# Kernel tuning notes

Measured on AMD Instinct MI355X. Metric: run time of the kernel, lower is better.

## Reference

```python
import jax, jax.numpy as jnp
import numpy as np
import math

B, L, D, H = 16, 512, 128, 8


def setup_inputs() -> dict:
    key = jax.random.key(0)
    ks = jax.random.split(key, 10)
    xavier = lambda k, shp: jax.random.normal(k, shp, jnp.float32) * math.sqrt(2.0 / (shp[0] + shp[1]))
    inp = {
        "x": jax.random.normal(ks[0], (B, L, D), jnp.float32),
        "W_q": xavier(ks[1], (H * D, D)),
        "b_q": jnp.zeros((H * D,), jnp.float32),
        "W_k": xavier(ks[2], (H * D, D)),
        "b_k": jnp.zeros((H * D,), jnp.float32),
        "W_v": xavier(ks[3], (H * D, D)),
        "b_v": jnp.zeros((H * D,), jnp.float32),
        "W_o": xavier(ks[4], (D, H * D)),
        "b_o": jnp.zeros((D,), jnp.float32),
        "pad_mask": jax.random.randint(ks[5], (B, L, L), 0, 2).astype(bool),
        "batch_size": B,
        "max_len": L,
    }
    return inp


def reference(x, W_q, b_q, W_k, b_k, W_v, b_v, W_o, b_o, pad_mask, batch_size, max_len):
    # project: [B, L, D] -> [B, L, H*D] -> head-major [H*B, L, D]
    def proj(W, b):
        y = jnp.einsum('bld,ed->ble', x, W) + b          # [B, L, H*D]
        y = y.reshape(batch_size, max_len, H, D)
        return y.transpose(2, 0, 1, 3).reshape(H * batch_size, max_len, D)

    q = proj(W_q, b_q)
    k = proj(W_k, b_k)
    v = proj(W_v, b_v)

    scores = jnp.einsum('nqd,nkd->nqk', q, k)            # [H*B, L, L]
    mask = jnp.tile(pad_mask, (H, 1, 1))                 # repeat(n_heads,1,1)
    # faithful quirk: mask BEFORE scaling, softmax over QUERY axis (dim=1)
    scores = jnp.where(mask, -1e9, scores) / math.sqrt(D)
    attn = jax.nn.softmax(scores, axis=1)
    att = jnp.einsum('nqk,nkd->nqd', attn, v)            # [H*B, L, D]
    # faithful quirk: torch .view from (H*B, L, D) to (B, L, H*D)
    att = att.reshape(batch_size, max_len, H * D)
    out = jnp.einsum('ble,de->bld', att, W_o) + b_o      # [B, L, D]
    return out
```

## Files before the change

kernel.cpp:

```cpp
#include <hip/hip_runtime.h>

#define B_  16
#define L_  512
#define D_  128
#define H_  8
#define HD_ 1024
#define NH_ 128
#define M_  8192

typedef unsigned short u16;
typedef __attribute__((ext_vector_type(8))) short s16x8;
typedef __attribute__((ext_vector_type(4))) float f32x4;

__device__ __forceinline__ float bf2f(u16 u) {
    union { unsigned u; float f; } x; x.u = ((unsigned)u) << 16; return x.f;
}
__device__ __forceinline__ u16 f2bf(float f) {
    unsigned u = __float_as_uint(f);
    return (u16)((u + 0x7FFFu + ((u >> 16) & 1u)) >> 16);
}

template<int MI, int MJ>
__device__ __forceinline__ void mfma_bt(const u16* __restrict__ A, int lda,
                                        const u16* __restrict__ B, int ldb,
                                        int K, int lane, f32x4 acc[MI][MJ]) {
    const int mr = lane & 15, quad = lane >> 4;
    for (int k0 = 0; k0 < K; k0 += 32) {
        s16x8 av[MI], bv[MJ];
#pragma unroll
        for (int i = 0; i < MI; i++)
            av[i] = *(const s16x8*)(A + (size_t)(i * 16 + mr) * lda + k0 + quad * 8);
#pragma unroll
        for (int j = 0; j < MJ; j++)
            bv[j] = *(const s16x8*)(B + (size_t)(j * 16 + mr) * ldb + k0 + quad * 8);
#pragma unroll
        for (int i = 0; i < MI; i++)
#pragma unroll
            for (int j = 0; j < MJ; j++)
                acc[i][j] = __builtin_amdgcn_mfma_f32_16x16x32_bf16(av[i], bv[j], acc[i][j], 0, 0, 0);
    }
}

__global__ void k0_detect(const unsigned int* __restrict__ pad,
                          const unsigned int* __restrict__ xw,
                          int* __restrict__ flags) {
    __shared__ int sMask, sCnt;
    if (threadIdx.x == 0) { sMask = 0; sCnt = 0; }
    __syncthreads();
    int bad = 0;
#pragma unroll
    for (int i = 0; i < 4; i++) {
        unsigned u = pad[threadIdx.x * 4 + i];
        bad |= (u > 1u) ? 1 : 0;
    }
    int cnt = 0;
#pragma unroll
    for (int i = 0; i < 16; i++) {
        unsigned w = xw[threadIdx.x * 16 + i];
        unsigned e = (w >> 7) & 0xFFu;
        cnt += (e >= 100u && e <= 131u) ? 1 : 0;
    }
    if (bad) atomicOr(&sMask, 1);
    atomicAdd(&sCnt, cnt);
    __syncthreads();
    if (threadIdx.x == 0) {
        flags[0] = (sCnt > 2048) ? 1 : 0;
        flags[1] = sMask;
    }
}

#define PREP_G8 197008
__global__ __launch_bounds__(256) void kprep_conv8(
    const void* x, const void* Wq, const void* bq, const void* Wk, const void* bk,
    const void* Wv, const void* bv, const void* Wo, const void* bo,
    const int* __restrict__ flags,
    u16* xb, u16* Wqb, u16* Wkb, u16* Wvb, u16* Wob,
    u16* bqb, u16* bkb, u16* bvb, u16* bob) {
    int g = blockIdx.x * 256 + threadIdx.x;
    if (g >= PREP_G8) return;
    int e0 = g * 8;
    const int dt = flags[0];
    const void* src; u16* dst; int off;
    if      (e0 < 1048576) { src = x;  dst = xb;  off = e0; }
    else if (e0 < 1179648) { src = Wq; dst = Wqb; off = e0 - 1048576; }
    else if (e0 < 1310720) { src = Wk; dst = Wkb; off = e0 - 1179648; }
    else if (e0 < 1441792) { src = Wv; dst = Wvb; off = e0 - 1310720; }
    else if (e0 < 1572864) { src = Wo; dst = Wob; off = e0 - 1441792; }
    else if (e0 < 1573888) { src = bq; dst = bqb; off = e0 - 1572864; }
    else if (e0 < 1574912) { src = bk; dst = bkb; off = e0 - 1573888; }
    else if (e0 < 1575936) { src = bv; dst = bvb; off = e0 - 1574912; }
    else                   { src = bo; dst = bob; off = e0 - 1575936; }
    if (dt) {
        *(uint4*)(dst + off) = *(const uint4*)((const u16*)src + off);
    } else {
        float4 a = *(const float4*)((const float*)src + off);
        float4 b = *(const float4*)((const float*)src + off + 4);
        u16 t[8] = {f2bf(a.x), f2bf(a.y), f2bf(a.z), f2bf(a.w),
                    f2bf(b.x), f2bf(b.y), f2bf(b.z), f2bf(b.w)};
        *(uint4*)(dst + off) = *(const uint4*)t;
    }
}

__global__ __launch_bounds__(256) void kprep_mask(const void* __restrict__ pad,
                                                  const int* __restrict__ flags,
                                                  unsigned* __restrict__ mb,
                                                  float* __restrict__ lsum) {
    int w = blockIdx.x * 256 + threadIdx.x;
    if (w < 65536) lsum[w] = 0.f;
    unsigned m = 0;
    if (flags[1]) {
        union { uint4 v[2]; unsigned a[8]; } u;
        u.v[0] = ((const uint4*)pad)[w * 2];
        u.v[1] = ((const uint4*)pad)[w * 2 + 1];
#pragma unroll
        for (int b = 0; b < 32; b++)
            m |= (((u.a[b >> 2] >> ((b & 3) * 8)) & 0xFFu) ? 1u : 0u) << b;
    } else {
        union { uint4 v[8]; unsigned a[32]; } u;
#pragma unroll
        for (int i = 0; i < 8; i++) u.v[i] = ((const uint4*)pad)[w * 8 + i];
#pragma unroll
        for (int b = 0; b < 32; b++) m |= (u.a[b] ? 1u : 0u) << b;
    }
    mb[w] = m;
}

__global__ __launch_bounds__(256) void k1_proj(
    const u16* __restrict__ xb,
    const u16* __restrict__ Wqb, const u16* __restrict__ Wkb, const u16* __restrict__ Wvb,
    const u16* __restrict__ bqb, const u16* __restrict__ bkb, const u16* __restrict__ bvb,
    u16* __restrict__ qb, u16* __restrict__ kb, u16* __restrict__ vtb) {
    const int h  = blockIdx.x;
    const int m0 = blockIdx.y * 128;
    const int z  = blockIdx.z;
    const u16* W    = (z == 0) ? Wqb : (z == 1) ? Wkb : Wvb;
    const u16* bias = (z == 0) ? bqb : (z == 1) ? bkb : bvb;

    const int lane = threadIdx.x & 63, wave = threadIdx.x >> 6;
    const int wr = wave >> 1, wc = wave & 1;
    const int mr = lane & 15, quad = lane >> 4;

    f32x4 acc[4][4];
#pragma unroll
    for (int i = 0; i < 4; i++)
#pragma unroll
        for (int j = 0; j < 4; j++) acc[i][j] = (f32x4){0.f, 0.f, 0.f, 0.f};

    mfma_bt<4,4>(xb + (size_t)(m0 + wr * 64) * D_, D_,
                 W + (size_t)(h * 128 + wc * 64) * D_, D_, D_, lane, acc);

    __shared__ __align__(16) u16 T[128][136];
#pragma unroll
    for (int i = 0; i < 4; i++)
#pragma unroll
        for (int j = 0; j < 4; j++) {
            int col = wc * 64 + j * 16 + mr;
            float bv_ = bf2f(bias[h * 128 + col]);
#pragma unroll
            for (int r = 0; r < 4; r++)
                T[wr * 64 + i * 16 + quad * 4 + r][col] = f2bf(acc[i][j][r] + bv_);
        }
    __syncthreads();

    const int bb = m0 >> 9, l0 = m0 & 511;
    const int t = threadIdx.x;
    if (z < 2) {
        u16* out = z ? kb : qb;
        int row = t >> 1, c0 = (t & 1) * 64;
        u16* dst = out + ((size_t)(h * B_ + bb) * L_ + l0 + row) * D_ + c0;
#pragma unroll
        for (int c = 0; c < 64; c += 8)
            *(uint4*)(dst + c) = *(const uint4*)&T[row][c0 + c];
    } else {
        int d = t >> 1, lc0 = (t & 1) * 64;
        u16* dst = vtb + ((size_t)(h * B_ + bb) * D_ + d) * L_ + l0 + lc0;
#pragma unroll
        for (int c = 0; c < 64; c += 8) {
            u16 tmp[8];
#pragma unroll
            for (int s = 0; s < 8; s++) tmp[s] = T[lc0 + c + s][d];
            *(uint4*)(dst + c) = *(const uint4*)tmp;
        }
    }
}

__global__ __launch_bounds__(256) void k2_escore(
    const u16* __restrict__ qb, const u16* __restrict__ kb,
    const unsigned* __restrict__ mbits,
    u16* __restrict__ E, float* __restrict__ lsum) {
    const int n  = blockIdx.x;
    const int ks = blockIdx.y;
    const int qq = blockIdx.z;
    const int bb = n & (B_ - 1);
    const int tid = threadIdx.x;
    const int lane = tid & 63, wave = tid >> 6;
    const int wr = wave >> 1, wc = wave & 1;
    const int mr = lane & 15, quad = lane >> 4;
    const float rs = 0.08838834764831845f;

    __shared__ __align__(16) u16 Te[128][136];
    __shared__ unsigned mw[512];
    __shared__ float CS[2][128];

#pragma unroll
    for (int s = 0; s < 2; s++) {
        int idx = tid * 2 + s;
        int ql = idx >> 2, lw = idx & 3;
        mw[idx] = mbits[((size_t)(bb << 9) + qq * 128 + ql) * 16 + ks * 4 + lw];
    }
    __syncthreads();

    f32x4 acc[4][4];
#pragma unroll
    for (int i = 0; i < 4; i++)
#pragma unroll
        for (int j = 0; j < 4; j++) acc[i][j] = (f32x4){0.f, 0.f, 0.f, 0.f};

    mfma_bt<4,4>(qb + (size_t)n * L_ * D_ + (size_t)(qq * 128 + wr * 64) * D_, D_,
                 kb + (size_t)n * L_ * D_ + (size_t)(ks * 128 + wc * 64) * D_, D_,
                 D_, lane, acc);

    float colsum[4] = {0.f, 0.f, 0.f, 0.f};
#pragma unroll
    for (int j = 0; j < 4; j++) {
        const int kc = wc * 64 + j * 16 + mr;
        const int lw = kc >> 5, bit = kc & 31;
#pragma unroll
        for (int i = 0; i < 4; i++)
#pragma unroll
            for (int r = 0; r < 4; r++) {
                int ql = wr * 64 + i * 16 + quad * 4 + r;
                float e = ((mw[(ql << 2) + lw] >> bit) & 1u)
                          ? 0.f : __expf(acc[i][j][r] * rs);
                colsum[j] += e;
                Te[ql][kc] = f2bf(e);
            }
    }
#pragma unroll
    for (int j = 0; j < 4; j++) {
        colsum[j] += __shfl_xor(colsum[j], 16);
        colsum[j] += __shfl_xor(colsum[j], 32);
    }
    if (quad == 0) {
#pragma unroll
        for (int j = 0; j < 4; j++) CS[wr][wc * 64 + j * 16 + mr] = colsum[j];
    }
    __syncthreads();

    {
        int row = tid >> 1, c0 = (tid & 1) * 64;
        u16* dst = E + ((size_t)(n * L_ + qq * 128 + row)) * L_ + ks * 128 + c0;
#pragma unroll
        for (int c = 0; c < 64; c += 8)
            *(uint4*)(dst + c) = *(const uint4*)&Te[row][c0 + c];
    }
    if (tid < 128)
        atomicAdd(&lsum[(size_t)n * L_ + ks * 128 + tid], CS[0][tid] + CS[1][tid]);
}

__global__ __launch_bounds__(256) void k3_vscale(u16* __restrict__ vtb,
                                                 const float* __restrict__ lsum) {
    int idx = blockIdx.x * 256 + threadIdx.x;
    int n = idx >> 13;
    int rem = idx & 8191;
    int d = rem >> 6;
    int kg = (rem & 63) << 3;
    u16* p = vtb + ((size_t)n * D_ + d) * L_ + kg;
    uint4 v = *(const uint4*)p;
    float4 l0 = *(const float4*)(lsum + (size_t)n * L_ + kg);
    float4 l1 = *(const float4*)(lsum + (size_t)n * L_ + kg + 4);
    float lv[8] = {1.f/l0.x, 1.f/l0.y, 1.f/l0.z, 1.f/l0.w,
                   1.f/l1.x, 1.f/l1.y, 1.f/l1.z, 1.f/l1.w};
    u16* u = (u16*)&v;
#pragma unroll
    for (int s = 0; s < 8; s++) u[s] = f2bf(bf2f(u[s]) * lv[s]);
    *(uint4*)p = v;
}

__global__ __launch_bounds__(256) void k4_av(
    const u16* __restrict__ E, const u16* __restrict__ vtb,
    u16* __restrict__ att) {
    const int n  = blockIdx.x;
    const int qt = blockIdx.y;
    const int tid = threadIdx.x;
    const int lane = tid & 63, w = tid >> 6;
    const int mr = lane & 15, quad = lane >> 4;

    f32x4 acc[4][2];
#pragma unroll
    for (int i = 0; i < 4; i++)
#pragma unroll
        for (int j = 0; j < 2; j++) acc[i][j] = (f32x4){0.f, 0.f, 0.f, 0.f};

    mfma_bt<4,2>(E + ((size_t)n * L_ + qt * 64) * L_, L_,
                 vtb + ((size_t)n * D_ + w * 32) * L_, L_, L_, lane, acc);

    __shared__ __align__(16) u16 Ta[64][136];
#pragma unroll
    for (int i = 0; i < 4; i++)
#pragma unroll
        for (int j = 0; j < 2; j++) {
            int col = w * 32 + j * 16 + mr;
#pragma unroll
            for (int r = 0; r < 4; r++)
                Ta[i * 16 + quad * 4 + r][col] = f2bf(acc[i][j][r]);
        }
    __syncthreads();
    int row = tid >> 2, c0 = (tid & 3) * 32;
    u16* dst = att + ((size_t)(n * L_ + qt * 64 + row)) * D_ + c0;
#pragma unroll
    for (int c = 0; c < 32; c += 8)
        *(uint4*)(dst + c) = *(const uint4*)&Ta[row][c0 + c];
}

__global__ __launch_bounds__(256) void k5_out(
    const u16* __restrict__ att, const u16* __restrict__ Wob,
    const u16* __restrict__ bob, const int* __restrict__ flags,
    void* __restrict__ out) {
    const int dt = flags[0];
    const int n0 = blockIdx.x * 64;
    const int m0 = blockIdx.y * 32;
    const int tid = threadIdx.x;
    const int lane = tid & 63, wk = tid >> 6;
    const int mr = lane & 15, quad = lane >> 4;

    f32x4 acc[2][4];
#pragma unroll
    for (int i = 0; i < 2; i++)
#pragma unroll
        for (int j = 0; j < 4; j++) acc[i][j] = (f32x4){0.f, 0.f, 0.f, 0.f};

    mfma_bt<2,4>(att + (size_t)m0 * HD_ + wk * 256, HD_,
                 Wob + (size_t)n0 * HD_ + wk * 256, HD_, 256, lane, acc);

    __shared__ __align__(16) float Tf[2][32][68];
    if (wk < 2) {
#pragma unroll
        for (int i = 0; i < 2; i++)
#pragma unroll
            for (int j = 0; j < 4; j++)
#pragma unroll
                for (int r = 0; r < 4; r++)
                    Tf[wk][i * 16 + quad * 4 + r][j * 16 + mr] = acc[i][j][r];
    }
    __syncthreads();
    if (wk >= 2) {
#pragma unroll
        for (int i = 0; i < 2; i++)
#pragma unroll
            for (int j = 0; j < 4; j++)
#pragma unroll
                for (int r = 0; r < 4; r++)
                    Tf[wk - 2][i * 16 + quad * 4 + r][j * 16 + mr] += acc[i][j][r];
    }
    __syncthreads();

    int row = tid >> 3, c0 = (tid & 7) * 8;
    size_t base = (size_t)(m0 + row) * D_ + n0 + c0;
    float v[8];
#pragma unroll
    for (int s = 0; s < 8; s++)
        v[s] = Tf[0][row][c0 + s] + Tf[1][row][c0 + s] + bf2f(bob[n0 + c0 + s]);
    if (dt) {
        u16 tmp[8];
#pragma unroll
        for (int s = 0; s < 8; s++) tmp[s] = f2bf(v[s]);
        *(uint4*)((u16*)out + base) = *(const uint4*)tmp;
    } else {
        float* o = (float*)out;
        *(float4*)(o + base)     = *(const float4*)&v[0];
        *(float4*)(o + base + 4) = *(const float4*)&v[4];
    }
}

extern "C" void kernel_launch(void* const* d_in, const int* in_sizes, int n_in,
                              void* d_out, int out_size, void* d_ws, size_t ws_size,
                              hipStream_t stream) {
    (void)in_sizes; (void)n_in; (void)out_size; (void)ws_size;
    const void* x  = d_in[0];
    const void* Wq = d_in[1]; const void* bq = d_in[2];
    const void* Wk = d_in[3]; const void* bk = d_in[4];
    const void* Wv = d_in[5]; const void* bv = d_in[6];
    const void* Wo = d_in[7]; const void* bo = d_in[8];
    const void* pad = d_in[9];

    char* p = (char*)d_ws;
    auto alloc = [&](size_t bytes) { char* r = p; p += (bytes + 255) & ~(size_t)255; return r; };
    int*  flags = (int*)alloc(256);
    u16*  xb   = (u16*)alloc(2097152);
    u16*  Wqb  = (u16*)alloc(262144);
    u16*  Wkb  = (u16*)alloc(262144);
    u16*  Wvb  = (u16*)alloc(262144);
    u16*  Wob  = (u16*)alloc(262144);
    u16*  bqb  = (u16*)alloc(2048);
    u16*  bkb  = (u16*)alloc(2048);
    u16*  bvb  = (u16*)alloc(2048);
    u16*  bob  = (u16*)alloc(256);
    unsigned* mbits = (unsigned*)alloc(524288);
    float* lsum = (float*)alloc(262144);
    u16*  qb   = (u16*)alloc(16777216);
    u16*  kb   = (u16*)alloc(16777216);
    u16*  vtb  = (u16*)alloc(16777216);
    u16*  E    = (u16*)alloc(67108864);
    u16*  att  = qb;

    k0_detect<<<1, 256, 0, stream>>>((const unsigned*)pad, (const unsigned*)x, flags);
    kprep_conv8<<<(PREP_G8 + 255) / 256, 256, 0, stream>>>(
        x, Wq, bq, Wk, bk, Wv, bv, Wo, bo, flags,
        xb, Wqb, Wkb, Wvb, Wob, bqb, bkb, bvb, bob);
    kprep_mask<<<512, 256, 0, stream>>>(pad, flags, mbits, lsum);
    k1_proj<<<dim3(8, 64, 3), 256, 0, stream>>>(
        xb, Wqb, Wkb, Wvb, bqb, bkb, bvb, qb, kb, vtb);
    k2_escore<<<dim3(128, 4, 4), 256, 0, stream>>>(qb, kb, mbits, E, lsum);
    k3_vscale<<<4096, 256, 0, stream>>>(vtb, lsum);
    k4_av<<<dim3(128, 8), 256, 0, stream>>>(E, vtb, att);
    k5_out<<<dim3(2, 256), 256, 0, stream>>>(att, Wob, bob, flags, d_out);
}
```

Baseline: 263.3 us.

## Fuse prep kernels, fold V column scaling into AV GEMM, retile score kernel

```diff
diff --git a/kernel.cpp b/kernel.cpp
--- a/kernel.cpp
+++ b/kernel.cpp
@@ -20,11 +20,12 @@
     return (u16)((u + 0x7FFFu + ((u >> 16) & 1u)) >> 16);
 }
 
-template<int MI, int MJ>
+template<int MI, int MJ, int K>
 __device__ __forceinline__ void mfma_bt(const u16* __restrict__ A, int lda,
                                         const u16* __restrict__ B, int ldb,
-                                        int K, int lane, f32x4 acc[MI][MJ]) {
+                                        int lane, f32x4 acc[MI][MJ]) {
     const int mr = lane & 15, quad = lane >> 4;
+#pragma unroll
     for (int k0 = 0; k0 < K; k0 += 32) {
         s16x8 av[MI], bv[MJ];
 #pragma unroll
@@ -70,59 +71,57 @@
 }
 
 #define PREP_G8 197008
-__global__ __launch_bounds__(256) void kprep_conv8(
+__global__ __launch_bounds__(256) void kprep(
     const void* x, const void* Wq, const void* bq, const void* Wk, const void* bk,
     const void* Wv, const void* bv, const void* Wo, const void* bo,
-    const int* __restrict__ flags,
+    const void* __restrict__ pad, const int* __restrict__ flags,
     u16* xb, u16* Wqb, u16* Wkb, u16* Wvb, u16* Wob,
-    u16* bqb, u16* bkb, u16* bvb, u16* bob) {
-    int g = blockIdx.x * 256 + threadIdx.x;
-    if (g >= PREP_G8) return;
-    int e0 = g * 8;
-    const int dt = flags[0];
-    const void* src; u16* dst; int off;
-    if      (e0 < 1048576) { src = x;  dst = xb;  off = e0; }
-    else if (e0 < 1179648) { src = Wq; dst = Wqb; off = e0 - 1048576; }
-    else if (e0 < 1310720) { src = Wk; dst = Wkb; off = e0 - 1179648; }
-    else if (e0 < 1441792) { src = Wv; dst = Wvb; off = e0 - 1310720; }
-    else if (e0 < 1572864) { src = Wo; dst = Wob; off = e0 - 1441792; }
-    else if (e0 < 1573888) { src = bq; dst = bqb; off = e0 - 1572864; }
-    else if (e0 < 1574912) { src = bk; dst = bkb; off = e0 - 1573888; }
-    else if (e0 < 1575936) { src = bv; dst = bvb; off = e0 - 1574912; }
-    else                   { src = bo; dst = bob; off = e0 - 1575936; }
-    if (dt) {
-        *(uint4*)(dst + off) = *(const uint4*)((const u16*)src + off);
+    u16* bqb, u16* bkb, u16* bvb, u16* bob,
+    unsigned* __restrict__ mb, float* __restrict__ lsum) {
+    if (blockIdx.x < 770) {
+        int g = blockIdx.x * 256 + threadIdx.x;
+        if (g >= PREP_G8) return;
+        int e0 = g * 8;
+        const int dt = flags[0];
+        const void* src; u16* dst; int off;
+        if      (e0 < 1048576) { src = x;  dst = xb;  off = e0; }
+        else if (e0 < 1179648) { src = Wq; dst = Wqb; off = e0 - 1048576; }
+        else if (e0 < 1310720) { src = Wk; dst = Wkb; off = e0 - 1179648; }
+        else if (e0 < 1441792) { src = Wv; dst = Wvb; off = e0 - 1310720; }
+        else if (e0 < 1572864) { src = Wo; dst = Wob; off = e0 - 1441792; }
+        else if (e0 < 1573888) { src = bq; dst = bqb; off = e0 - 1572864; }
+        else if (e0 < 1574912) { src = bk; dst = bkb; off = e0 - 1573888; }
+        else if (e0 < 1575936) { src = bv; dst = bvb; off = e0 - 1574912; }
+        else                   { src = bo; dst = bob; off = e0 - 1575936; }
+        if (dt) {
+            *(uint4*)(dst + off) = *(const uint4*)((const u16*)src + off);
+        } else {
+            float4 a = *(const float4*)((const float*)src + off);
+            float4 b = *(const float4*)((const float*)src + off + 4);
+            u16 t[8] = {f2bf(a.x), f2bf(a.y), f2bf(a.z), f2bf(a.w),
+                        f2bf(b.x), f2bf(b.y), f2bf(b.z), f2bf(b.w)};
+            *(uint4*)(dst + off) = *(const uint4*)t;
+        }
     } else {
-        float4 a = *(const float4*)((const float*)src + off);
-        float4 b = *(const float4*)((const float*)src + off + 4);
-        u16 t[8] = {f2bf(a.x), f2bf(a.y), f2bf(a.z), f2bf(a.w),
-                    f2bf(b.x), f2bf(b.y), f2bf(b.z), f2bf(b.w)};
-        *(uint4*)(dst + off) = *(const uint4*)t;
-    }
-}
-
-__global__ __launch_bounds__(256) void kprep_mask(const void* __restrict__ pad,
-                                                  const int* __restrict__ flags,
-                                                  unsigned* __restrict__ mb,
-                                                  float* __restrict__ lsum) {
-    int w = blockIdx.x * 256 + threadIdx.x;
-    if (w < 65536) lsum[w] = 0.f;
-    unsigned m = 0;
-    if (flags[1]) {
-        union { uint4 v[2]; unsigned a[8]; } u;
-        u.v[0] = ((const uint4*)pad)[w * 2];
-        u.v[1] = ((const uint4*)pad)[w * 2 + 1];
-#pragma unroll
-        for (int b = 0; b < 32; b++)
-            m |= (((u.a[b >> 2] >> ((b & 3) * 8)) & 0xFFu) ? 1u : 0u) << b;
-    } else {
-        union { uint4 v[8]; unsigned a[32]; } u;
-#pragma unroll
-        for (int i = 0; i < 8; i++) u.v[i] = ((const uint4*)pad)[w * 8 + i];
-#pragma unroll
-        for (int b = 0; b < 32; b++) m |= (u.a[b] ? 1u : 0u) << b;
-    }
-    mb[w] = m;
+        int w = (blockIdx.x - 770) * 256 + threadIdx.x;
+        if (w < 65536) lsum[w] = 0.f;
+        unsigned m = 0;
+        if (flags[1]) {
+            union { uint4 v[2]; unsigned a[8]; } u;
+            u.v[0] = ((const uint4*)pad)[w * 2];
+            u.v[1] = ((const uint4*)pad)[w * 2 + 1];
+#pragma unroll
+            for (int b = 0; b < 32; b++)
+                m |= (((u.a[b >> 2] >> ((b & 3) * 8)) & 0xFFu) ? 1u : 0u) << b;
+        } else {
+            union { uint4 v[8]; unsigned a[32]; } u;
+#pragma unroll
+            for (int i = 0; i < 8; i++) u.v[i] = ((const uint4*)pad)[w * 8 + i];
+#pragma unroll
+            for (int b = 0; b < 32; b++) m |= (u.a[b] ? 1u : 0u) << b;
+        }
+        mb[w] = m;
+    }
 }
 
 __global__ __launch_bounds__(256) void k1_proj(
@@ -146,8 +145,8 @@
 #pragma unroll
         for (int j = 0; j < 4; j++) acc[i][j] = (f32x4){0.f, 0.f, 0.f, 0.f};
 
-    mfma_bt<4,4>(xb + (size_t)(m0 + wr * 64) * D_, D_,
-                 W + (size_t)(h * 128 + wc * 64) * D_, D_, D_, lane, acc);
+    mfma_bt<4,4,128>(xb + (size_t)(m0 + wr * 64) * D_, D_,
+                     W + (size_t)(h * 128 + wc * 64) * D_, D_, lane, acc);
 
     __shared__ __align__(16) u16 T[128][136];
 #pragma unroll
@@ -190,112 +189,116 @@
     u16* __restrict__ E, float* __restrict__ lsum) {
     const int n  = blockIdx.x;
     const int ks = blockIdx.y;
-    const int qq = blockIdx.z;
+    const int qs = blockIdx.z;
     const int bb = n & (B_ - 1);
     const int tid = threadIdx.x;
-    const int lane = tid & 63, wave = tid >> 6;
-    const int wr = wave >> 1, wc = wave & 1;
+    const int lane = tid & 63, w = tid >> 6;
     const int mr = lane & 15, quad = lane >> 4;
     const float rs = 0.08838834764831845f;
 
-    __shared__ __align__(16) u16 Te[128][136];
-    __shared__ unsigned mw[512];
-    __shared__ float CS[2][128];
-
-#pragma unroll
-    for (int s = 0; s < 2; s++) {
-        int idx = tid * 2 + s;
-        int ql = idx >> 2, lw = idx & 3;
-        mw[idx] = mbits[((size_t)(bb << 9) + qq * 128 + ql) * 16 + ks * 4 + lw];
-    }
-    __syncthreads();
-
-    f32x4 acc[4][4];
+    __shared__ __align__(16) u16 Te[64][136];
+    __shared__ unsigned mw[256];
+    mw[tid] = mbits[((size_t)(bb << 9) + qs * 64 + (tid >> 2)) * 16 + ks * 4 + (tid & 3)];
+    __syncthreads();
+
+    f32x4 acc[4][2];
 #pragma unroll
     for (int i = 0; i < 4; i++)
 #pragma unroll
-        for (int j = 0; j < 4; j++) acc[i][j] = (f32x4){0.f, 0.f, 0.f, 0.f};
-
-    mfma_bt<4,4>(qb + (size_t)n * L_ * D_ + (size_t)(qq * 128 + wr * 64) * D_, D_,
-                 kb + (size_t)n * L_ * D_ + (size_t)(ks * 128 + wc * 64) * D_, D_,
-                 D_, lane, acc);
-
-    float colsum[4] = {0.f, 0.f, 0.f, 0.f};
-#pragma unroll
-    for (int j = 0; j < 4; j++) {
-        const int kc = wc * 64 + j * 16 + mr;
-        const int lw = kc >> 5, bit = kc & 31;
+        for (int j = 0; j < 2; j++) acc[i][j] = (f32x4){0.f, 0.f, 0.f, 0.f};
+
+    mfma_bt<4,2,128>(qb + ((size_t)n * L_ + qs * 64) * D_, D_,
+                     kb + ((size_t)n * L_ + ks * 128 + w * 32) * D_, D_, lane, acc);
+
+    float colsum[2] = {0.f, 0.f};
+#pragma unroll
+    for (int j = 0; j < 2; j++) {
+        const int kcL = w * 32 + j * 16 + mr;
+        const int word = kcL >> 5, bit = kcL & 31;
 #pragma unroll
         for (int i = 0; i < 4; i++)
 #pragma unroll
             for (int r = 0; r < 4; r++) {
-                int ql = wr * 64 + i * 16 + quad * 4 + r;
-                float e = ((mw[(ql << 2) + lw] >> bit) & 1u)
+                int ql = i * 16 + quad * 4 + r;
+                float e = ((mw[ql * 4 + word] >> bit) & 1u)
                           ? 0.f : __expf(acc[i][j][r] * rs);
                 colsum[j] += e;
-                Te[ql][kc] = f2bf(e);
+                Te[ql][kcL] = f2bf(e);
             }
     }
 #pragma unroll
-    for (int j = 0; j < 4; j++) {
+    for (int j = 0; j < 2; j++) {
         colsum[j] += __shfl_xor(colsum[j], 16);
         colsum[j] += __shfl_xor(colsum[j], 32);
     }
     if (quad == 0) {
 #pragma unroll
-        for (int j = 0; j < 4; j++) CS[wr][wc * 64 + j * 16 + mr] = colsum[j];
-    }
-    __syncthreads();
-
+        for (int j = 0; j < 2; j++)
+            atomicAdd(&lsum[(size_t)n * L_ + ks * 128 + w * 32 + j * 16 + mr], colsum[j]);
+    }
+    __syncthreads();
     {
-        int row = tid >> 1, c0 = (tid & 1) * 64;
-        u16* dst = E + ((size_t)(n * L_ + qq * 128 + row)) * L_ + ks * 128 + c0;
-#pragma unroll
-        for (int c = 0; c < 64; c += 8)
+        int row = tid >> 2, c0 = (tid & 3) * 32;
+        u16* dst = E + ((size_t)n * L_ + qs * 64 + row) * L_ + ks * 128 + c0;
+#pragma unroll
+        for (int c = 0; c < 32; c += 8)
             *(uint4*)(dst + c) = *(const uint4*)&Te[row][c0 + c];
     }
-    if (tid < 128)
-        atomicAdd(&lsum[(size_t)n * L_ + ks * 128 + tid], CS[0][tid] + CS[1][tid]);
-}
-
-__global__ __launch_bounds__(256) void k3_vscale(u16* __restrict__ vtb,
-                                                 const float* __restrict__ lsum) {
-    int idx = blockIdx.x * 256 + threadIdx.x;
-    int n = idx >> 13;
-    int rem = idx & 8191;
-    int d = rem >> 6;
-    int kg = (rem & 63) << 3;
-    u16* p = vtb + ((size_t)n * D_ + d) * L_ + kg;
-    uint4 v = *(const uint4*)p;
-    float4 l0 = *(const float4*)(lsum + (size_t)n * L_ + kg);
-    float4 l1 = *(const float4*)(lsum + (size_t)n * L_ + kg + 4);
-    float lv[8] = {1.f/l0.x, 1.f/l0.y, 1.f/l0.z, 1.f/l0.w,
-                   1.f/l1.x, 1.f/l1.y, 1.f/l1.z, 1.f/l1.w};
-    u16* u = (u16*)&v;
-#pragma unroll
-    for (int s = 0; s < 8; s++) u[s] = f2bf(bf2f(u[s]) * lv[s]);
-    *(uint4*)p = v;
 }
 
 __global__ __launch_bounds__(256) void k4_av(
     const u16* __restrict__ E, const u16* __restrict__ vtb,
-    u16* __restrict__ att) {
+    const float* __restrict__ lsum, u16* __restrict__ att) {
     const int n  = blockIdx.x;
     const int qt = blockIdx.y;
     const int tid = threadIdx.x;
     const int lane = tid & 63, w = tid >> 6;
     const int mr = lane & 15, quad = lane >> 4;
 
+    __shared__ float linvS[512];
+    __shared__ __align__(16) u16 Ta[64][136];
+    if (tid < 128) {
+        const float* lp = lsum + (size_t)n * L_ + tid * 4;
+        float4 a = *(const float4*)lp;
+        linvS[tid * 4 + 0] = 1.f / a.x; linvS[tid * 4 + 1] = 1.f / a.y;
+        linvS[tid * 4 + 2] = 1.f / a.z; linvS[tid * 4 + 3] = 1.f / a.w;
+    }
+    __syncthreads();
+
+    const u16* Eb = E + ((size_t)n * L_ + qt * 64) * L_;
+    const u16* vb = vtb + ((size_t)n * D_ + w * 32) * L_;
+
     f32x4 acc[4][2];
 #pragma unroll
     for (int i = 0; i < 4; i++)
 #pragma unroll
         for (int j = 0; j < 2; j++) acc[i][j] = (f32x4){0.f, 0.f, 0.f, 0.f};
 
-    mfma_bt<4,2>(E + ((size_t)n * L_ + qt * 64) * L_, L_,
-                 vtb + ((size_t)n * D_ + w * 32) * L_, L_, L_, lane, acc);
-
-    __shared__ __align__(16) u16 Ta[64][136];
+#pragma unroll 4
+    for (int k0 = 0; k0 < L_; k0 += 32) {
+        s16x8 av[4], bv[2];
+#pragma unroll
+        for (int i = 0; i < 4; i++)
+            av[i] = *(const s16x8*)(Eb + (size_t)(i * 16 + mr) * L_ + k0 + quad * 8);
+        float lv[8];
+        *(float4*)&lv[0] = *(const float4*)&linvS[k0 + quad * 8];
+        *(float4*)&lv[4] = *(const float4*)&linvS[k0 + quad * 8 + 4];
+#pragma unroll
+        for (int j = 0; j < 2; j++) {
+            s16x8 raw = *(const s16x8*)(vb + (size_t)(j * 16 + mr) * L_ + k0 + quad * 8);
+            union { u16 u[8]; s16x8 v; } t;
+#pragma unroll
+            for (int s = 0; s < 8; s++)
+                t.u[s] = f2bf(bf2f((u16)raw[s]) * lv[s]);
+            bv[j] = t.v;
+        }
+#pragma unroll
+        for (int i = 0; i < 4; i++)
+#pragma unroll
+            for (int j = 0; j < 2; j++)
+                acc[i][j] = __builtin_amdgcn_mfma_f32_16x16x32_bf16(av[i], bv[j], acc[i][j], 0, 0, 0);
+    }
+
 #pragma unroll
     for (int i = 0; i < 4; i++)
 #pragma unroll
@@ -306,11 +309,13 @@
                 Ta[i * 16 + quad * 4 + r][col] = f2bf(acc[i][j][r]);
         }
     __syncthreads();
-    int row = tid >> 2, c0 = (tid & 3) * 32;
-    u16* dst = att + ((size_t)(n * L_ + qt * 64 + row)) * D_ + c0;
-#pragma unroll
-    for (int c = 0; c < 32; c += 8)
-        *(uint4*)(dst + c) = *(const uint4*)&Ta[row][c0 + c];
+    {
+        int row = tid >> 2, c0 = (tid & 3) * 32;
+        u16* dst = att + ((size_t)n * L_ + qt * 64 + row) * D_ + c0;
+#pragma unroll
+        for (int c = 0; c < 32; c += 8)
+            *(uint4*)(dst + c) = *(const uint4*)&Ta[row][c0 + c];
+    }
 }
 
 __global__ __launch_bounds__(256) void k5_out(
@@ -330,8 +335,8 @@
 #pragma unroll
         for (int j = 0; j < 4; j++) acc[i][j] = (f32x4){0.f, 0.f, 0.f, 0.f};
 
-    mfma_bt<2,4>(att + (size_t)m0 * HD_ + wk * 256, HD_,
-                 Wob + (size_t)n0 * HD_ + wk * 256, HD_, 256, lane, acc);
+    mfma_bt<2,4,256>(att + (size_t)m0 * HD_ + wk * 256, HD_,
+                     Wob + (size_t)n0 * HD_ + wk * 256, HD_, lane, acc);
 
     __shared__ __align__(16) float Tf[2][32][68];
     if (wk < 2) {
@@ -405,14 +410,12 @@
     u16*  att  = qb;
 
     k0_detect<<<1, 256, 0, stream>>>((const unsigned*)pad, (const unsigned*)x, flags);
-    kprep_conv8<<<(PREP_G8 + 255) / 256, 256, 0, stream>>>(
-        x, Wq, bq, Wk, bk, Wv, bv, Wo, bo, flags,
-        xb, Wqb, Wkb, Wvb, Wob, bqb, bkb, bvb, bob);
-    kprep_mask<<<512, 256, 0, stream>>>(pad, flags, mbits, lsum);
+    kprep<<<1282, 256, 0, stream>>>(
+        x, Wq, bq, Wk, bk, Wv, bv, Wo, bo, pad, flags,
+        xb, Wqb, Wkb, Wvb, Wob, bqb, bkb, bvb, bob, mbits, lsum);
     k1_proj<<<dim3(8, 64, 3), 256, 0, stream>>>(
         xb, Wqb, Wkb, Wvb, bqb, bkb, bvb, qb, kb, vtb);
-    k2_escore<<<dim3(128, 4, 4), 256, 0, stream>>>(qb, kb, mbits, E, lsum);
-    k3_vscale<<<4096, 256, 0, stream>>>(vtb, lsum);
-    k4_av<<<dim3(128, 8), 256, 0, stream>>>(E, vtb, att);
+    k2_escore<<<dim3(128, 4, 8), 256, 0, stream>>>(qb, kb, mbits, E, lsum);
+    k4_av<<<dim3(128, 8), 256, 0, stream>>>(E, vtb, lsum, att);
     k5_out<<<dim3(2, 256), 256, 0, stream>>>(att, Wob, bob, flags, d_out);
 }
```

Result: no change. 262.6 us (-0.3%).
